# Optimization experiments

Hardware: AMD Instinct MI355X
Metric: run time of the kernel (lower is better)

## Reference

```python
import jax, jax.numpy as jnp
import numpy as np

B, S, HID = 1, 2048, 4096
H, HKV, DFULL, D = 32, 8, 128, 96
GROUPS = H // HKV
SCALE = DFULL ** -0.5  # scaling uses the FULL head_dim per the source
ROPE_THETA = 10000.0


def setup_inputs() -> dict:
    key = jax.random.key(0)
    ks = jax.random.split(key, 8)
    hidden_states = jax.random.normal(ks[0], (B, S, HID), jnp.float32)
    # standard HF Llama RoPE tables over the FULL head dim
    inv_freq = 1.0 / (ROPE_THETA ** (jnp.arange(0, DFULL, 2, dtype=jnp.float32) / DFULL))
    ang = jnp.arange(S, dtype=jnp.float32)[:, None] * inv_freq[None, :]  # [S, DFULL/2]
    emb = jnp.concatenate([ang, ang], axis=-1)  # [S, DFULL]
    cos = jnp.cos(emb)[None]  # [1, S, DFULL]
    sin = jnp.sin(emb)[None]
    # per-kv-head frequency indices: lo half in [0, DFULL/2), hi half = lo + DFULL/2
    half, dh = DFULL // 2, D // 2
    idx_lo = jax.random.randint(ks[1], (HKV, dh), 0, half)
    indices = jnp.concatenate([idx_lo, idx_lo + half], axis=-1).astype(jnp.int32)  # [HKV, D]
    s = 0.02
    Wq = jax.random.normal(ks[2], (H * D, HID), jnp.float32) * s
    Wk = jax.random.normal(ks[3], (HKV * D, HID), jnp.float32) * s
    Wv = jax.random.normal(ks[4], (HKV * D, HID), jnp.float32) * s
    Wo = jax.random.normal(ks[5], (HID, H * D), jnp.float32) * s
    return {"hidden_states": hidden_states, "cos": cos, "sin": sin,
            "indices": indices, "Wq": Wq, "Wk": Wk, "Wv": Wv, "Wo": Wo}


def rotate_half(x):
    x1, x2 = jnp.split(x, 2, axis=-1)
    return jnp.concatenate([-x2, x1], axis=-1)


def reference(hidden_states, cos, sin, indices, Wq, Wk, Wv, Wo):
    b, s, _ = hidden_states.shape
    # QKV projections (no bias), reshape to [B, heads, S, D]
    q = (hidden_states @ Wq.T).reshape(b, s, H, D).transpose(0, 2, 1, 3)
    k = (hidden_states @ Wk.T).reshape(b, s, HKV, D).transpose(0, 2, 1, 3)
    v = (hidden_states @ Wv.T).reshape(b, s, HKV, D).transpose(0, 2, 1, 3)
    # indexed RoPE: gather per-kv-head frequencies from the full-dim tables
    cos_h = cos[:, :, indices].transpose(0, 2, 1, 3)  # [B, HKV, S, D]
    sin_h = sin[:, :, indices].transpose(0, 2, 1, 3)
    cos_q = jnp.repeat(cos_h, GROUPS, axis=1)  # [B, H, S, D]
    sin_q = jnp.repeat(sin_h, GROUPS, axis=1)
    q = q * cos_q + rotate_half(q) * sin_q
    k = k * cos_h + rotate_half(k) * sin_h
    # GQA: repeat kv to num_attention_heads
    k = jnp.repeat(k, GROUPS, axis=1)  # [B, H, S, D]
    v = jnp.repeat(v, GROUPS, axis=1)
    scores = jnp.einsum('bhqd,bhkd->bhqk', q, k) * SCALE
    causal = jnp.tril(jnp.ones((s, s), dtype=bool))
    scores = jnp.where(causal[None, None], scores, jnp.finfo(scores.dtype).min)
    probs = jax.nn.softmax(scores, axis=-1)
    out = jnp.einsum('bhqk,bhkd->bhqd', probs, v)  # [B, H, S, D]
    out = out.transpose(0, 2, 1, 3).reshape(b, s, H * D)
    return out @ Wo.T
```

## Files before the change

### kernel.cpp

```cpp
#include <hip/hip_runtime.h>

typedef unsigned short u16;
typedef unsigned int u32;
typedef __bf16 bf16x8 __attribute__((ext_vector_type(8)));
typedef float f32x4 __attribute__((ext_vector_type(4)));

#define SCALE_Q2 0.12751743443398106f

#define GLDS16(gp, lp)                                                        \
  __builtin_amdgcn_global_load_lds(                                           \
      (const __attribute__((address_space(1))) void*)(gp),                    \
      (__attribute__((address_space(3))) void*)(lp), 16, 0, 0)

__device__ __forceinline__ u16 f2bf(float f) {
  u32 u = __builtin_bit_cast(u32, f);
  u += 0x7fffu + ((u >> 16) & 1u);
  return (u16)(u >> 16);
}
__device__ __forceinline__ float bf2f(u16 b) {
  u32 u = ((u32)b) << 16;
  return __builtin_bit_cast(float, u);
}

__global__ __launch_bounds__(256) void cvt_kernel(const float* __restrict__ src,
                                                  u16* __restrict__ dst, int n4) {
  int i = blockIdx.x * 256 + threadIdx.x;
  if (i >= n4) return;
  float4 v = ((const float4*)src)[i];
  u32 lo = (u32)f2bf(v.x) | ((u32)f2bf(v.y) << 16);
  u32 hi = (u32)f2bf(v.z) | ((u32)f2bf(v.w) << 16);
  ((uint2*)dst)[i] = make_uint2(lo, hi);
}

template <bool BF16OUT>
__global__ __launch_bounds__(256) void gemm_bt(const u16* __restrict__ A,
                                               const u16* __restrict__ B,
                                               void* __restrict__ Cout,
                                               int M, int N, int K) {
  __shared__ u16 As[128 * 64];
  __shared__ u16 Bs[128 * 64];
  const int tid = threadIdx.x;
  const int w = tid >> 6, lane = tid & 63, quad = lane >> 4, c16 = lane & 15;
  const int m0 = blockIdx.y * 128, n0 = blockIdx.x * 128;
  const int wm = (w & 1) * 64, wn = (w >> 1) * 64;
  const int srow8 = lane >> 3;
  const int scg = (lane & 7) ^ srow8;

  f32x4 acc[4][4];
#pragma unroll
  for (int i = 0; i < 4; i++)
#pragma unroll
    for (int j = 0; j < 4; j++) acc[i][j] = (f32x4){0.f, 0.f, 0.f, 0.f};

  const u16* Abase = A + (size_t)(m0 + w * 8 + srow8) * K + scg * 8;
  const u16* Bbase = B + (size_t)(n0 + w * 8 + srow8) * K + scg * 8;

  for (int k0 = 0; k0 < K; k0 += 64) {
    __syncthreads();
#pragma unroll
    for (int it = 0; it < 4; it++) {
      GLDS16(Abase + (size_t)(it * 32) * K + k0, &As[(w * 8 + it * 32) * 64]);
      GLDS16(Bbase + (size_t)(it * 32) * K + k0, &Bs[(w * 8 + it * 32) * 64]);
    }
    __syncthreads();
#pragma unroll
    for (int kk = 0; kk < 2; kk++) {
      bf16x8 af[4], bf[4];
#pragma unroll
      for (int mt = 0; mt < 4; mt++) {
        int row = wm + mt * 16 + c16;
        int col = (kk * 4 + quad) ^ (row & 7);
        af[mt] = *(const bf16x8*)(&As[row * 64 + col * 8]);
      }
#pragma unroll
      for (int nt = 0; nt < 4; nt++) {
        int row = wn + nt * 16 + c16;
        int col = (kk * 4 + quad) ^ (row & 7);
        bf[nt] = *(const bf16x8*)(&Bs[row * 64 + col * 8]);
      }
#pragma unroll
      for (int mt = 0; mt < 4; mt++)
#pragma unroll
        for (int nt = 0; nt < 4; nt++)
          acc[mt][nt] = __builtin_amdgcn_mfma_f32_16x16x32_bf16(af[mt], bf[nt], acc[mt][nt], 0, 0, 0);
    }
  }
#pragma unroll
  for (int mt = 0; mt < 4; mt++)
#pragma unroll
    for (int nt = 0; nt < 4; nt++)
#pragma unroll
      for (int r = 0; r < 4; r++) {
        int m = m0 + wm + mt * 16 + quad * 4 + r;
        int n = n0 + wn + nt * 16 + c16;
        if (BF16OUT)
          ((u16*)Cout)[(size_t)m * N + n] = f2bf(acc[mt][nt][r]);
        else
          ((float*)Cout)[(size_t)m * N + n] = acc[mt][nt][r];
      }
}

__global__ __launch_bounds__(256) void rope_kernel(const u16* __restrict__ qkv,
                                                   const float* __restrict__ cosb,
                                                   const float* __restrict__ sinb,
                                                   const int* __restrict__ idxs,
                                                   u16* __restrict__ qB,
                                                   u16* __restrict__ kB) {
  u32 i = blockIdx.x * 256u + threadIdx.x;
  const u32 NQ = 2048u * 32u * 96u;
  if (i < NQ) {
    u32 s = i / 3072u, rem = i % 3072u;
    u32 h = rem / 96u, d = rem % 96u;
    u32 hkv = h >> 2;
    u32 base = s * 4608u + h * 96u + d;
    float x = bf2f(qkv[base]);
    float pv = (d < 48u) ? -bf2f(qkv[base + 48u]) : bf2f(qkv[base - 48u]);
    int idx = idxs[hkv * 96u + d];
    float c = cosb[s * 128u + idx], sn = sinb[s * 128u + idx];
    qB[(h * 2048u + s) * 96u + d] = f2bf((x * c + pv * sn) * SCALE_Q2);
  } else {
    u32 j = i - NQ;
    u32 s = j / 768u, rem = j % 768u;
    u32 hkv = rem / 96u, d = rem % 96u;
    u32 base = s * 4608u + 3072u + hkv * 96u + d;
    float x = bf2f(qkv[base]);
    float pv = (d < 48u) ? -bf2f(qkv[base + 48u]) : bf2f(qkv[base - 48u]);
    int idx = idxs[hkv * 96u + d];
    float c = cosb[s * 128u + idx], sn = sinb[s * 128u + idx];
    kB[(hkv * 2048u + s) * 96u + d] = f2bf(x * c + pv * sn);
  }
}

__global__ __launch_bounds__(256) void vtrans_kernel(const u16* __restrict__ qkvB,
                                                     u16* __restrict__ vtB) {
  __shared__ u16 T[64 * 34];
  const int s0 = blockIdx.x * 64, d0 = blockIdx.y * 32;
  const int tx = threadIdx.x & 31, ty = threadIdx.x >> 5;
#pragma unroll
  for (int it = 0; it < 8; it++) {
    int row = it * 8 + ty;
    T[row * 34 + tx] = qkvB[(size_t)(s0 + row) * 4608 + 3840 + d0 + tx];
  }
  __syncthreads();
  const int sx = threadIdx.x & 63, dy = threadIdx.x >> 6;
#pragma unroll
  for (int it = 0; it < 8; it++) {
    int d = it * 4 + dy;
    vtB[(size_t)(d0 + d) * 2048 + s0 + sx] = T[sx * 34 + d];
  }
}

__global__ __launch_bounds__(256) void attn_kernel(const u16* __restrict__ qB,
                                                   const u16* __restrict__ kB,
                                                   const u16* __restrict__ vtB,
                                                   u16* __restrict__ aoB) {
  __shared__ u16 Ks[64 * 96];
  __shared__ u16 Vs[96 * 64];
  __shared__ u16 Ps[4 * 16 * 64];
  const int tid = threadIdx.x;
  const int w = tid >> 6, lane = tid & 63, quad = lane >> 4, c16 = lane & 15;
  const int pr = blockIdx.x, h = blockIdx.y, hkv = h >> 2;
  u16* pw = Ps + w * (16 * 64);

  size_t voff[3];
#pragma unroll
  for (int it = 0; it < 3; it++) {
    int j = it * 256 + tid;
    int row = j >> 3, c = (j & 7) ^ (row & 7);
    voff[it] = (size_t)row * 2048 + c * 8;
  }
  const u16* kbase = kB + (size_t)hkv * 2048 * 96;
  const u16* vbase = vtB + (size_t)hkv * 96 * 2048;

  bf16x8 vones;
#pragma unroll
  for (int i = 0; i < 8; i++) vones[i] = (__bf16)1.0f;

  for (int ph = 0; ph < 2; ph++) {
    const int qt = ph ? (31 - pr) : pr;
    const int m_base = qt * 64 + w * 16;

    bf16x8 qf[3];
    {
      const u16* qrow = qB + ((size_t)h * 2048 + m_base + c16) * 96;
#pragma unroll
      for (int t = 0; t < 3; t++) qf[t] = *(const bf16x8*)(qrow + t * 32 + quad * 8);
    }
    f32x4 o[6], ol;
#pragma unroll
    for (int dt = 0; dt < 6; dt++) o[dt] = (f32x4){0.f, 0.f, 0.f, 0.f};
    ol = (f32x4){0.f, 0.f, 0.f, 0.f};

    for (int kt = 0; kt <= qt; kt++) {
      const int k0 = kt * 64;
      __syncthreads();
#pragma unroll
      for (int it = 0; it < 3; it++) {
        GLDS16(kbase + (size_t)k0 * 96 + (it * 256 + tid) * 8,
               &Ks[(it * 256 + w * 64) * 8]);
        GLDS16(vbase + voff[it] + k0, &Vs[(it * 256 + w * 64) * 8]);
      }
      __syncthreads();

      f32x4 sacc[4];
#pragma unroll
      for (int nt = 0; nt < 4; nt++) sacc[nt] = (f32x4){0.f, 0.f, 0.f, 0.f};
#pragma unroll
      for (int nt = 0; nt < 4; nt++)
#pragma unroll
        for (int t = 0; t < 3; t++) {
          bf16x8 kf = *(const bf16x8*)(&Ks[(nt * 16 + c16) * 96 + t * 32 + quad * 8]);
          sacc[nt] = __builtin_amdgcn_mfma_f32_16x16x32_bf16(qf[t], kf, sacc[nt], 0, 0, 0);
        }

      if (kt == qt) {
#pragma unroll
        for (int r = 0; r < 4; r++) {
          int row_abs = m_base + quad * 4 + r;
#pragma unroll
          for (int nt = 0; nt < 4; nt++)
            if (k0 + nt * 16 + c16 > row_abs) sacc[nt][r] = -__builtin_inff();
        }
      }

#pragma unroll
      for (int r = 0; r < 4; r++) {
        int mrow = quad * 4 + r, m7 = mrow & 7;
#pragma unroll
        for (int nt = 0; nt < 4; nt++) {
          float p = __builtin_amdgcn_exp2f(sacc[nt][r]);
          int chunk = (nt * 2 + (c16 >> 3)) ^ m7;
          pw[mrow * 64 + chunk * 8 + (c16 & 7)] =
              (u16)(__builtin_bit_cast(u32, p) >> 16);
        }
      }
      bf16x8 pf[2];
#pragma unroll
      for (int kti = 0; kti < 2; kti++) {
        int chunk = (kti * 4 + quad) ^ (c16 & 7);
        pf[kti] = *(const bf16x8*)(&pw[c16 * 64 + chunk * 8]);
      }
#pragma unroll
      for (int kti = 0; kti < 2; kti++) {
        ol = __builtin_amdgcn_mfma_f32_16x16x32_bf16(pf[kti], vones, ol, 0, 0, 0);
#pragma unroll
        for (int dt = 0; dt < 6; dt++) {
          int row = dt * 16 + c16;
          int vch = (kti * 4 + quad) ^ (row & 7);
          bf16x8 vf = *(const bf16x8*)(&Vs[row * 64 + vch * 8]);
          o[dt] = __builtin_amdgcn_mfma_f32_16x16x32_bf16(pf[kti], vf, o[dt], 0, 0, 0);
        }
      }
    }

#pragma unroll
    for (int r = 0; r < 4; r++) {
      float inv = 1.0f / ol[r];
      int row = m_base + quad * 4 + r;
#pragma unroll
      for (int dt = 0; dt < 6; dt++)
        aoB[(size_t)row * 3072 + h * 96 + dt * 16 + c16] = f2bf(o[dt][r] * inv);
    }
  }
}

extern "C" void kernel_launch(void* const* d_in, const int* in_sizes, int n_in,
                              void* d_out, int out_size, void* d_ws, size_t ws_size,
                              hipStream_t stream) {
  const float* hs   = (const float*)d_in[0];
  const float* cosb = (const float*)d_in[1];
  const float* sinb = (const float*)d_in[2];
  const int*   idxs = (const int*)d_in[3];
  const float* Wq   = (const float*)d_in[4];
  const float* Wk   = (const float*)d_in[5];
  const float* Wv   = (const float*)d_in[6];
  const float* Wo   = (const float*)d_in[7];
  float* out = (float*)d_out;
  char* ws = (char*)d_ws;

  u16* hsB   = (u16*)(ws);
  u16* wqkvB = (u16*)(ws + 16777216);
  u16* woB   = (u16*)(ws + 54525952);
  u16* qkvB  = (u16*)(ws + 79691776);
  u16* qB    = (u16*)(ws + 98566144);
  u16* kB    = (u16*)(ws + 111149056);
  u16* vtB   = (u16*)(ws + 114294784);
  u16* aoB   = (u16*)(ws + 117440512);

  cvt_kernel<<<8192, 256, 0, stream>>>(hs, hsB, 2097152);
  cvt_kernel<<<12288, 256, 0, stream>>>(Wq, wqkvB, 3145728);
  cvt_kernel<<<3072, 256, 0, stream>>>(Wk, wqkvB + 3072 * 4096, 786432);
  cvt_kernel<<<3072, 256, 0, stream>>>(Wv, wqkvB + 3840 * 4096, 786432);
  cvt_kernel<<<12288, 256, 0, stream>>>(Wo, woB, 3145728);

  gemm_bt<true><<<dim3(36, 16), 256, 0, stream>>>(hsB, wqkvB, qkvB, 2048, 4608, 4096);

  rope_kernel<<<30720, 256, 0, stream>>>(qkvB, cosb, sinb, idxs, qB, kB);
  vtrans_kernel<<<dim3(32, 24), 256, 0, stream>>>(qkvB, vtB);

  attn_kernel<<<dim3(16, 32), 256, 0, stream>>>(qB, kB, vtB, aoB);

  gemm_bt<false><<<dim3(32, 16), 256, 0, stream>>>(aoB, woB, out, 2048, 4096, 3072);
}
```

Before: 442.4 us.

## Fuse fp32-to-bf16 conversion into GEMM loads and double-buffer two-head attention

Removes the separate conversion kernels by having the GEMMs load fp32 inputs and weights directly and pack them to bf16 in LDS, with the QKV weights selected per block column. The attention kernel now processes two query heads per block sharing each K/V tile and prefetches the next K/V tile into a second LDS buffer. This cuts the extra conversion traffic and launches and overlaps loads with compute. In exchange, the GEMM staging becomes synchronous register loads of twice as many bytes, and attention launches half as many blocks with more registers per block.

```diff
diff --git a/kernel.cpp b/kernel.cpp
--- a/kernel.cpp
+++ b/kernel.cpp
@@ -21,47 +21,73 @@
   u32 u = ((u32)b) << 16;
   return __builtin_bit_cast(float, u);
 }
-
-__global__ __launch_bounds__(256) void cvt_kernel(const float* __restrict__ src,
-                                                  u16* __restrict__ dst, int n4) {
-  int i = blockIdx.x * 256 + threadIdx.x;
-  if (i >= n4) return;
-  float4 v = ((const float4*)src)[i];
-  u32 lo = (u32)f2bf(v.x) | ((u32)f2bf(v.y) << 16);
-  u32 hi = (u32)f2bf(v.z) | ((u32)f2bf(v.w) << 16);
-  ((uint2*)dst)[i] = make_uint2(lo, hi);
-}
-
-template <bool BF16OUT>
-__global__ __launch_bounds__(256) void gemm_bt(const u16* __restrict__ A,
-                                               const u16* __restrict__ B,
+__device__ __forceinline__ u32 pack2(float a, float b) {
+  u32 ua = __builtin_bit_cast(u32, a) + 0x8000u;
+  u32 ub = __builtin_bit_cast(u32, b) + 0x8000u;
+  return __builtin_amdgcn_perm(ub, ua, 0x07060302u);
+}
+
+__device__ __forceinline__ void stage_f32(const float* __restrict__ src,
+                                          int K, u16* lds, int tid) {
+  const int c = tid & 7, r0 = tid >> 3;
+#pragma unroll
+  for (int jr = 0; jr < 4; jr++) {
+    int row = r0 + jr * 32;
+    const float* p = src + (size_t)row * K + c * 8;
+    float4 lo = *(const float4*)p;
+    float4 hi = *(const float4*)(p + 4);
+    uint4 q = make_uint4(pack2(lo.x, lo.y), pack2(lo.z, lo.w),
+                         pack2(hi.x, hi.y), pack2(hi.z, hi.w));
+    int ch = c ^ (row & 7);
+    *(uint4*)(&lds[row * 64 + ch * 8]) = q;
+  }
+}
+
+template <bool AF32, bool BF16OUT, bool SPLIT>
+__global__ __launch_bounds__(256) void gemm_bt(const void* __restrict__ Ain,
+                                               const float* __restrict__ B0,
+                                               const float* __restrict__ B1,
+                                               const float* __restrict__ B2,
                                                void* __restrict__ Cout,
-                                               int M, int N, int K) {
+                                               int K, int ldc) {
   __shared__ u16 As[128 * 64];
   __shared__ u16 Bs[128 * 64];
   const int tid = threadIdx.x;
   const int w = tid >> 6, lane = tid & 63, quad = lane >> 4, c16 = lane & 15;
-  const int m0 = blockIdx.y * 128, n0 = blockIdx.x * 128;
+  const int bx = blockIdx.x;
+  const int m0 = blockIdx.y * 128, n0 = bx * 128;
   const int wm = (w & 1) * 64, wn = (w >> 1) * 64;
+
+  const float* Bp;
+  if (SPLIT) {
+    if (bx < 24)      Bp = B0 + (size_t)n0 * K;
+    else if (bx < 30) Bp = B1 + (size_t)(n0 - 3072) * K;
+    else              Bp = B2 + (size_t)(n0 - 3840) * K;
+  } else {
+    Bp = B0 + (size_t)n0 * K;
+  }
+
   const int srow8 = lane >> 3;
   const int scg = (lane & 7) ^ srow8;
+  const u16* Abf = (const u16*)Ain + (size_t)(m0 + w * 8 + srow8) * K + scg * 8;
+  const float* Af32 = (const float*)Ain + (size_t)m0 * K;
 
   f32x4 acc[4][4];
 #pragma unroll
   for (int i = 0; i < 4; i++)
 #pragma unroll
     for (int j = 0; j < 4; j++) acc[i][j] = (f32x4){0.f, 0.f, 0.f, 0.f};
-
-  const u16* Abase = A + (size_t)(m0 + w * 8 + srow8) * K + scg * 8;
-  const u16* Bbase = B + (size_t)(n0 + w * 8 + srow8) * K + scg * 8;
 
   for (int k0 = 0; k0 < K; k0 += 64) {
     __syncthreads();
-#pragma unroll
-    for (int it = 0; it < 4; it++) {
-      GLDS16(Abase + (size_t)(it * 32) * K + k0, &As[(w * 8 + it * 32) * 64]);
-      GLDS16(Bbase + (size_t)(it * 32) * K + k0, &Bs[(w * 8 + it * 32) * 64]);
-    }
+    if (AF32) {
+      stage_f32(Af32 + k0, K, As, tid);
+    } else {
+#pragma unroll
+      for (int it = 0; it < 4; it++)
+        GLDS16(Abf + (size_t)(it * 32) * K + k0, &As[(w * 8 + it * 32) * 64]);
+    }
+    stage_f32(Bp + k0, K, Bs, tid);
     __syncthreads();
 #pragma unroll
     for (int kk = 0; kk < 2; kk++) {
@@ -94,9 +120,9 @@
         int m = m0 + wm + mt * 16 + quad * 4 + r;
         int n = n0 + wn + nt * 16 + c16;
         if (BF16OUT)
-          ((u16*)Cout)[(size_t)m * N + n] = f2bf(acc[mt][nt][r]);
+          ((u16*)Cout)[(size_t)m * ldc + n] = f2bf(acc[mt][nt][r]);
         else
-          ((float*)Cout)[(size_t)m * N + n] = acc[mt][nt][r];
+          ((float*)Cout)[(size_t)m * ldc + n] = acc[mt][nt][r];
       }
 }
 
@@ -150,17 +176,17 @@
   }
 }
 
-__global__ __launch_bounds__(256) void attn_kernel(const u16* __restrict__ qB,
-                                                   const u16* __restrict__ kB,
-                                                   const u16* __restrict__ vtB,
-                                                   u16* __restrict__ aoB) {
-  __shared__ u16 Ks[64 * 96];
-  __shared__ u16 Vs[96 * 64];
-  __shared__ u16 Ps[4 * 16 * 64];
+__global__ __launch_bounds__(256, 2) void attn_kernel(const u16* __restrict__ qB,
+                                                      const u16* __restrict__ kB,
+                                                      const u16* __restrict__ vtB,
+                                                      u16* __restrict__ aoB) {
+  __shared__ u16 Ks[2][64 * 96];
+  __shared__ u16 Vs[2][96 * 64];
+  __shared__ u16 Ps[4][16 * 64];
   const int tid = threadIdx.x;
   const int w = tid >> 6, lane = tid & 63, quad = lane >> 4, c16 = lane & 15;
-  const int pr = blockIdx.x, h = blockIdx.y, hkv = h >> 2;
-  u16* pw = Ps + w * (16 * 64);
+  const int pr = blockIdx.x, hkv = blockIdx.y, z = blockIdx.z;
+  u16* pw = Ps[w];
 
   size_t voff[3];
 #pragma unroll
@@ -180,86 +206,110 @@
     const int qt = ph ? (31 - pr) : pr;
     const int m_base = qt * 64 + w * 16;
 
-    bf16x8 qf[3];
-    {
+    bf16x8 qf[2][3];
+#pragma unroll
+    for (int hh = 0; hh < 2; hh++) {
+      int h = hkv * 4 + z * 2 + hh;
       const u16* qrow = qB + ((size_t)h * 2048 + m_base + c16) * 96;
 #pragma unroll
-      for (int t = 0; t < 3; t++) qf[t] = *(const bf16x8*)(qrow + t * 32 + quad * 8);
-    }
-    f32x4 o[6], ol;
-#pragma unroll
-    for (int dt = 0; dt < 6; dt++) o[dt] = (f32x4){0.f, 0.f, 0.f, 0.f};
-    ol = (f32x4){0.f, 0.f, 0.f, 0.f};
+      for (int t = 0; t < 3; t++) qf[hh][t] = *(const bf16x8*)(qrow + t * 32 + quad * 8);
+    }
+    f32x4 o[2][6], ol[2];
+#pragma unroll
+    for (int hh = 0; hh < 2; hh++) {
+      ol[hh] = (f32x4){0.f, 0.f, 0.f, 0.f};
+#pragma unroll
+      for (int dt = 0; dt < 6; dt++) o[hh][dt] = (f32x4){0.f, 0.f, 0.f, 0.f};
+    }
 
     for (int kt = 0; kt <= qt; kt++) {
+      const int cur = kt & 1;
+      if (kt == 0) {
+        __syncthreads();
+#pragma unroll
+        for (int it = 0; it < 3; it++) {
+          GLDS16(kbase + (size_t)0 * 96 + (it * 256 + tid) * 8,
+                 &Ks[0][(it * 256 + w * 64) * 8]);
+          GLDS16(vbase + voff[it] + 0, &Vs[0][(it * 256 + w * 64) * 8]);
+        }
+      }
+      __syncthreads();
+      if (kt < qt) {
+        const int k1 = (kt + 1) * 64;
+#pragma unroll
+        for (int it = 0; it < 3; it++) {
+          GLDS16(kbase + (size_t)k1 * 96 + (it * 256 + tid) * 8,
+                 &Ks[cur ^ 1][(it * 256 + w * 64) * 8]);
+          GLDS16(vbase + voff[it] + k1, &Vs[cur ^ 1][(it * 256 + w * 64) * 8]);
+        }
+      }
       const int k0 = kt * 64;
-      __syncthreads();
-#pragma unroll
-      for (int it = 0; it < 3; it++) {
-        GLDS16(kbase + (size_t)k0 * 96 + (it * 256 + tid) * 8,
-               &Ks[(it * 256 + w * 64) * 8]);
-        GLDS16(vbase + voff[it] + k0, &Vs[(it * 256 + w * 64) * 8]);
-      }
-      __syncthreads();
-
-      f32x4 sacc[4];
-#pragma unroll
-      for (int nt = 0; nt < 4; nt++) sacc[nt] = (f32x4){0.f, 0.f, 0.f, 0.f};
-#pragma unroll
-      for (int nt = 0; nt < 4; nt++)
-#pragma unroll
-        for (int t = 0; t < 3; t++) {
-          bf16x8 kf = *(const bf16x8*)(&Ks[(nt * 16 + c16) * 96 + t * 32 + quad * 8]);
-          sacc[nt] = __builtin_amdgcn_mfma_f32_16x16x32_bf16(qf[t], kf, sacc[nt], 0, 0, 0);
-        }
-
-      if (kt == qt) {
+
+#pragma unroll
+      for (int hh = 0; hh < 2; hh++) {
+        f32x4 sacc[4];
+#pragma unroll
+        for (int nt = 0; nt < 4; nt++) sacc[nt] = (f32x4){0.f, 0.f, 0.f, 0.f};
+#pragma unroll
+        for (int nt = 0; nt < 4; nt++)
+#pragma unroll
+          for (int t = 0; t < 3; t++) {
+            bf16x8 kf = *(const bf16x8*)(&Ks[cur][(nt * 16 + c16) * 96 + t * 32 + quad * 8]);
+            sacc[nt] = __builtin_amdgcn_mfma_f32_16x16x32_bf16(qf[hh][t], kf, sacc[nt], 0, 0, 0);
+          }
+
+        if (kt == qt) {
+#pragma unroll
+          for (int r = 0; r < 4; r++) {
+            int row_abs = m_base + quad * 4 + r;
+#pragma unroll
+            for (int nt = 0; nt < 4; nt++)
+              if (k0 + nt * 16 + c16 > row_abs) sacc[nt][r] = -__builtin_inff();
+          }
+        }
+
 #pragma unroll
         for (int r = 0; r < 4; r++) {
-          int row_abs = m_base + quad * 4 + r;
-#pragma unroll
-          for (int nt = 0; nt < 4; nt++)
-            if (k0 + nt * 16 + c16 > row_abs) sacc[nt][r] = -__builtin_inff();
-        }
-      }
-
+          int mrow = quad * 4 + r, m7 = mrow & 7;
+#pragma unroll
+          for (int nt = 0; nt < 4; nt++) {
+            float p = __builtin_amdgcn_exp2f(sacc[nt][r]);
+            int chunk = (nt * 2 + (c16 >> 3)) ^ m7;
+            pw[mrow * 64 + chunk * 8 + (c16 & 7)] =
+                (u16)(__builtin_bit_cast(u32, p) >> 16);
+          }
+        }
+        bf16x8 pf[2];
+#pragma unroll
+        for (int kti = 0; kti < 2; kti++) {
+          int chunk = (kti * 4 + quad) ^ (c16 & 7);
+          pf[kti] = *(const bf16x8*)(&pw[c16 * 64 + chunk * 8]);
+        }
+#pragma unroll
+        for (int kti = 0; kti < 2; kti++) {
+          ol[hh] = __builtin_amdgcn_mfma_f32_16x16x32_bf16(pf[kti], vones, ol[hh], 0, 0, 0);
+#pragma unroll
+          for (int dt = 0; dt < 6; dt++) {
+            int row = dt * 16 + c16;
+            int vch = (kti * 4 + quad) ^ (row & 7);
+            bf16x8 vf = *(const bf16x8*)(&Vs[cur][row * 64 + vch * 8]);
+            o[hh][dt] = __builtin_amdgcn_mfma_f32_16x16x32_bf16(pf[kti], vf, o[hh][dt], 0, 0, 0);
+          }
+        }
+      }
+    }
+
+#pragma unroll
+    for (int hh = 0; hh < 2; hh++) {
+      int h = hkv * 4 + z * 2 + hh;
 #pragma unroll
       for (int r = 0; r < 4; r++) {
-        int mrow = quad * 4 + r, m7 = mrow & 7;
-#pragma unroll
-        for (int nt = 0; nt < 4; nt++) {
-          float p = __builtin_amdgcn_exp2f(sacc[nt][r]);
-          int chunk = (nt * 2 + (c16 >> 3)) ^ m7;
-          pw[mrow * 64 + chunk * 8 + (c16 & 7)] =
-              (u16)(__builtin_bit_cast(u32, p) >> 16);
-        }
-      }
-      bf16x8 pf[2];
-#pragma unroll
-      for (int kti = 0; kti < 2; kti++) {
-        int chunk = (kti * 4 + quad) ^ (c16 & 7);
-        pf[kti] = *(const bf16x8*)(&pw[c16 * 64 + chunk * 8]);
-      }
-#pragma unroll
-      for (int kti = 0; kti < 2; kti++) {
-        ol = __builtin_amdgcn_mfma_f32_16x16x32_bf16(pf[kti], vones, ol, 0, 0, 0);
-#pragma unroll
-        for (int dt = 0; dt < 6; dt++) {
-          int row = dt * 16 + c16;
-          int vch = (kti * 4 + quad) ^ (row & 7);
-          bf16x8 vf = *(const bf16x8*)(&Vs[row * 64 + vch * 8]);
-          o[dt] = __builtin_amdgcn_mfma_f32_16x16x32_bf16(pf[kti], vf, o[dt], 0, 0, 0);
-        }
-      }
-    }
-
-#pragma unroll
-    for (int r = 0; r < 4; r++) {
-      float inv = 1.0f / ol[r];
-      int row = m_base + quad * 4 + r;
-#pragma unroll
-      for (int dt = 0; dt < 6; dt++)
-        aoB[(size_t)row * 3072 + h * 96 + dt * 16 + c16] = f2bf(o[dt][r] * inv);
+        float inv = 1.0f / ol[hh][r];
+        int row = m_base + quad * 4 + r;
+#pragma unroll
+        for (int dt = 0; dt < 6; dt++)
+          aoB[(size_t)row * 3072 + h * 96 + dt * 16 + c16] = f2bf(o[hh][dt][r] * inv);
+      }
     }
   }
 }
@@ -278,27 +328,20 @@
   float* out = (float*)d_out;
   char* ws = (char*)d_ws;
 
-  u16* hsB   = (u16*)(ws);
-  u16* wqkvB = (u16*)(ws + 16777216);
-  u16* woB   = (u16*)(ws + 54525952);
-  u16* qkvB  = (u16*)(ws + 79691776);
-  u16* qB    = (u16*)(ws + 98566144);
-  u16* kB    = (u16*)(ws + 111149056);
-  u16* vtB   = (u16*)(ws + 114294784);
-  u16* aoB   = (u16*)(ws + 117440512);
-
-  cvt_kernel<<<8192, 256, 0, stream>>>(hs, hsB, 2097152);
-  cvt_kernel<<<12288, 256, 0, stream>>>(Wq, wqkvB, 3145728);
-  cvt_kernel<<<3072, 256, 0, stream>>>(Wk, wqkvB + 3072 * 4096, 786432);
-  cvt_kernel<<<3072, 256, 0, stream>>>(Wv, wqkvB + 3840 * 4096, 786432);
-  cvt_kernel<<<12288, 256, 0, stream>>>(Wo, woB, 3145728);
-
-  gemm_bt<true><<<dim3(36, 16), 256, 0, stream>>>(hsB, wqkvB, qkvB, 2048, 4608, 4096);
+  u16* qkvB = (u16*)(ws);
+  u16* qB   = (u16*)(ws + 18874368);
+  u16* kB   = (u16*)(ws + 31457280);
+  u16* vtB  = (u16*)(ws + 34603008);
+  u16* aoB  = (u16*)(ws + 37748736);
+
+  gemm_bt<true, true, true><<<dim3(36, 16), 256, 0, stream>>>(
+      hs, Wq, Wk, Wv, qkvB, 4096, 4608);
 
   rope_kernel<<<30720, 256, 0, stream>>>(qkvB, cosb, sinb, idxs, qB, kB);
   vtrans_kernel<<<dim3(32, 24), 256, 0, stream>>>(qkvB, vtB);
 
-  attn_kernel<<<dim3(16, 32), 256, 0, stream>>>(qB, kB, vtB, aoB);
-
-  gemm_bt<false><<<dim3(32, 16), 256, 0, stream>>>(aoB, woB, out, 2048, 4096, 3072);
-}
+  attn_kernel<<<dim3(16, 8, 2), 256, 0, stream>>>(qB, kB, vtB, aoB);
+
+  gemm_bt<false, false, false><<<dim3(32, 16), 256, 0, stream>>>(
+      aoB, Wo, nullptr, nullptr, out, 3072, 4096);
+}
```

New measurement: 561.5 us. 26.9% more time.
